# Kernel optimization log

Measured on AMD Instinct MI355X. Metric: run time of the kernel, lower is better.

Reference implementation:

```python
import jax, jax.numpy as jnp
import numpy as np

B, C, H, W = 4, 512, 32, 32
NUM_HEADS, DIM_HEAD = 16, 32
DIM_ATTN = NUM_HEADS * DIM_HEAD  # 512
N = H * W


def setup_inputs() -> dict:
    key = jax.random.key(0)
    ks = jax.random.split(key, 6)
    s = 0.02
    return {
        "x": jax.random.normal(ks[0], (B, C, H, W), jnp.float32),
        "w_qkv": jax.random.normal(ks[1], (3 * DIM_ATTN, C), jnp.float32) * s,
        "b_qkv": jax.random.normal(ks[2], (3 * DIM_ATTN,), jnp.float32) * s,
        "w_proj": jax.random.normal(ks[3], (C, DIM_ATTN), jnp.float32) * s,
        "b_proj": jax.random.normal(ks[4], (C,), jnp.float32) * s,
        "shared_rel_pos": jax.random.normal(ks[5], (1, NUM_HEADS, N, N), jnp.float32) * s,
    }


def reference(x, w_qkv, b_qkv, w_proj, b_proj, shared_rel_pos):
    b, c, h, w = x.shape
    n = h * w
    scale = DIM_HEAD ** -0.5
    # 1x1 conv == per-pixel matmul over channels
    qkv = jnp.einsum('bchw,oc->bohw', x, w_qkv) + b_qkv[None, :, None, None]
    # [B, heads, 3*dh, N] -> chunk along dim 2 (matches torch .chunk(3, dim=2))
    qkv = qkv.reshape(b, NUM_HEADS, 3 * DIM_HEAD, n)
    q, k, v = jnp.split(qkv, 3, axis=2)          # each [B, heads, dh, N]
    attn = jnp.einsum('bhdi,bhdj->bhij', q, k) * scale  # q^T @ k
    attn = attn + shared_rel_pos
    attn = jax.nn.softmax(attn, axis=-1)
    out = jnp.einsum('bhdj,bhij->bhdi', v, attn)  # v @ attn^T, [B, heads, dh, N]
    out = out.reshape(b, NUM_HEADS * DIM_HEAD, h, w)
    out = jnp.einsum('bchw,oc->bohw', out, w_proj) + b_proj[None, :, None, None]
    return out
```

## Files before the change

### kernel.cpp

```cpp
#include <hip/hip_runtime.h>
#include <cstdint>
#include <cstddef>

#define BATCH 4
#define CIN   512
#define NPIX  1024
#define HEADS 16
#define DH    32
#define DATTN 512
#define O_QKV 1536

typedef unsigned short u16;
typedef __bf16 bf16x4 __attribute__((ext_vector_type(4)));
typedef __bf16 bf16x8 __attribute__((ext_vector_type(8)));
typedef float  f32x4  __attribute__((ext_vector_type(4)));

typedef const __attribute__((address_space(1))) void g1_t;
typedef __attribute__((address_space(3))) void l3_t;

#if defined(__has_builtin)
#if __has_builtin(__builtin_amdgcn_exp2f)
#define EXP2(x) __builtin_amdgcn_exp2f(x)
#endif
#endif
#ifndef EXP2
#define EXP2(x) __expf((x) * 0.6931471805599453f)
#endif

__device__ __forceinline__ u16 f2bf(float f) {
  unsigned u = __float_as_uint(f);
  u += 0x7fffu + ((u >> 16) & 1u);
  return (u16)(u >> 16);
}

__device__ __forceinline__ void gl_lds16(const void* gp, void* lp) {
  __builtin_amdgcn_global_load_lds((g1_t*)gp, (l3_t*)lp, 16, 0, 0);
}

__global__ __launch_bounds__(256) void prep_fused(const float* __restrict__ x,
                                                  const float* __restrict__ w1,
                                                  const float* __restrict__ w2,
                                                  u16* __restrict__ xt,
                                                  u16* __restrict__ o1,
                                                  u16* __restrict__ o2) {
  const int t = threadIdx.x;
  if (blockIdx.x < 512) {
    __shared__ float sT[64][65];
    const int q  = blockIdx.x;
    const int n0 = (q & 15) << 6;
    const int c0 = ((q >> 4) & 7) << 6;
    const int b  = q >> 7;
    const float* xb = x + ((size_t)b * CIN + c0) * NPIX + n0;
#pragma unroll
    for (int i = 0; i < 4; ++i) {
      int r   = i * 16 + (t >> 4);
      int col = (t & 15) << 2;
      float4 v = *reinterpret_cast<const float4*>(&xb[(size_t)r * NPIX + col]);
      sT[r][col + 0] = v.x; sT[r][col + 1] = v.y;
      sT[r][col + 2] = v.z; sT[r][col + 3] = v.w;
    }
    __syncthreads();
#pragma unroll
    for (int i = 0; i < 2; ++i) {
      int nl = t >> 2;
      int ch = (t & 3) + (i << 2);
      u16 tmp[8];
#pragma unroll
      for (int e = 0; e < 8; ++e) tmp[e] = f2bf(sT[(ch << 3) + e][nl]);
      *reinterpret_cast<uint4*>(&xt[((size_t)b * NPIX + n0 + nl) * CIN + c0 + (ch << 3)]) =
          *reinterpret_cast<uint4*>(tmp);
    }
  } else {
    const int idx = (blockIdx.x - 512) * 256 + t;
    const int n1 = (O_QKV * CIN) >> 2;
    float4 v = (idx < n1) ? reinterpret_cast<const float4*>(w1)[idx]
                          : reinterpret_cast<const float4*>(w2)[idx - n1];
    uint2 pk = make_uint2((unsigned)f2bf(v.x) | ((unsigned)f2bf(v.y) << 16),
                          (unsigned)f2bf(v.z) | ((unsigned)f2bf(v.w) << 16));
    if (idx < n1) reinterpret_cast<uint2*>(o1)[idx] = pk;
    else          reinterpret_cast<uint2*>(o2)[idx - n1] = pk;
  }
}

__global__ __launch_bounds__(256) void gemm_qkv_mfma(const u16* __restrict__ wq,
                                                     const u16* __restrict__ xt,
                                                     const float* __restrict__ bias,
                                                     u16* __restrict__ qt,
                                                     u16* __restrict__ kt,
                                                     u16* __restrict__ vt) {
  __shared__ __align__(16) u16 sA[96 * 64];
  __shared__ __align__(16) u16 sB[128 * 64];
  const int t  = threadIdx.x;
  const int w  = t >> 6, l = t & 63, g = l >> 4, ln = l & 15;
  const int n0 = blockIdx.x * 128;
  const int h  = blockIdx.y;
  const int b  = blockIdx.z;
  const int wm = w >> 1, wn = w & 1;

  const u16* wbase = wq + (size_t)h * 96 * CIN;
  const u16* xbase = xt + ((size_t)b * NPIX + n0) * CIN;

  f32x4 acc[3][4];
#pragma unroll
  for (int mi = 0; mi < 3; ++mi)
#pragma unroll
    for (int ni = 0; ni < 4; ++ni) acc[mi][ni] = {0.f, 0.f, 0.f, 0.f};

  for (int k0 = 0; k0 < CIN; k0 += 64) {
#pragma unroll
    for (int i = 0; i < 3; ++i) {
      int chunk = i * 256 + (w << 6) + l;
      gl_lds16(wbase + ((size_t)(chunk >> 3)) * CIN + k0 + ((chunk & 7) << 3),
               (char*)sA + i * 4096 + (w << 10));
    }
#pragma unroll
    for (int i = 0; i < 4; ++i) {
      int chunk = i * 256 + (w << 6) + l;
      gl_lds16(xbase + ((size_t)(chunk >> 3)) * CIN + k0 + ((chunk & 7) << 3),
               (char*)sB + i * 4096 + (w << 10));
    }
    __syncthreads();
#pragma unroll
    for (int kk = 0; kk < 64; kk += 32) {
      bf16x8 af[3], bfr[4];
#pragma unroll
      for (int mi = 0; mi < 3; ++mi)
        af[mi] = *reinterpret_cast<const bf16x8*>(&sA[(48 * wm + 16 * mi + ln) * 64 + kk + (g << 3)]);
#pragma unroll
      for (int ni = 0; ni < 4; ++ni)
        bfr[ni] = *reinterpret_cast<const bf16x8*>(&sB[((wn << 6) + (ni << 4) + ln) * 64 + kk + (g << 3)]);
#pragma unroll
      for (int mi = 0; mi < 3; ++mi)
#pragma unroll
        for (int ni = 0; ni < 4; ++ni)
          acc[mi][ni] = __builtin_amdgcn_mfma_f32_16x16x32_bf16(af[mi], bfr[ni], acc[mi][ni], 0, 0, 0);
    }
    __syncthreads();
  }

  const float QSC = 0.17677669529663687f * 1.4426950408889634f;
  const float* bh = bias + h * 96;
#pragma unroll
  for (int mi = 0; mi < 3; ++mi) {
    const int sec = 48 * wm + 16 * mi;
    const int rb  = sec + (g << 2);
    const float b0 = bh[rb + 0], b1 = bh[rb + 1], b2 = bh[rb + 2], b3 = bh[rb + 3];
#pragma unroll
    for (int ni = 0; ni < 4; ++ni) {
      const int n = n0 + (wn << 6) + (ni << 4) + ln;
      f32x4 a = acc[mi][ni];
      float v0 = a[0] + b0, v1 = a[1] + b1, v2 = a[2] + b2, v3 = a[3] + b3;
      if (sec < 32) { v0 *= QSC; v1 *= QSC; v2 *= QSC; v3 *= QSC; }
      u16 e0 = f2bf(v0), e1 = f2bf(v1), e2 = f2bf(v2), e3 = f2bf(v3);
      if (sec < 32) {
        const int d = sec + (g << 2);
        uint2 pk = make_uint2((unsigned)e0 | ((unsigned)e1 << 16),
                              (unsigned)e2 | ((unsigned)e3 << 16));
        *reinterpret_cast<uint2*>(&qt[(((size_t)(b * HEADS + h)) * NPIX + n) * DH + d]) = pk;
      } else if (sec < 64) {
        const int d = sec - 32 + (g << 2);
        uint2 pk = make_uint2((unsigned)e0 | ((unsigned)e1 << 16),
                              (unsigned)e2 | ((unsigned)e3 << 16));
        *reinterpret_cast<uint2*>(&kt[(((size_t)(b * HEADS + h)) * NPIX + n) * DH + d]) = pk;
      } else {
        const int d = sec - 64 + (g << 2);
        u16* vp = &vt[(((size_t)(b * HEADS + h)) * DH + d) * NPIX + n];
        vp[0] = e0; vp[NPIX] = e1; vp[2 * NPIX] = e2; vp[3 * NPIX] = e3;
      }
    }
  }
}

__global__ __launch_bounds__(512, 4) void attn_mfma(const u16* __restrict__ qt,
                                                    const u16* __restrict__ kt,
                                                    const u16* __restrict__ vt,
                                                    const float* __restrict__ rel,
                                                    u16* __restrict__ aout) {
  __shared__ __align__(16) u16 sK[2][2][2][2048];
  __shared__ __align__(16) u16 sV[2][2][2][2048];
  __shared__ __align__(16) u16 sP[8][1024];

  const int t  = threadIdx.x;
  const int w  = t >> 6, l = t & 63, g = l >> 4, ln = l & 15;
  const int bid = blockIdx.x;
  const int xcd = bid & 7, sl = bid >> 3;
  const int bp  = sl & 1;
  const int i0  = ((sl >> 1) & 15) << 6;
  const int h   = (xcd << 1) | (sl >> 5);
  const int iw  = w & 3;
  const int jh  = w >> 2;

  const size_t bh0 = (size_t)((bp * 2 + 0) * HEADS + h);
  const size_t bh1 = (size_t)((bp * 2 + 1) * HEADS + h);

  const int sb2  = iw >> 1;
  const bool isK = (iw & 1) == 0;
  const size_t sbh = sb2 ? bh1 : bh0;
  const u16* src[4];
#pragma unroll
  for (int i = 0; i < 4; ++i) {
    const int c = i * 64 + l;
    const int r = c >> 3, slot = c & 7;
    if (isK) {
      const int kc = slot ^ (r & 7) ^ ((r >> 3) & 1);
      src[i] = kt + sbh * NPIX * DH +
               ((size_t)((jh << 9) + ((r << 1) | (kc >> 2)))) * DH + ((kc & 3) << 3);
    } else {
      const int vc = slot ^ (r & 7);
      src[i] = vt + (sbh * DH + r) * NPIX + (jh << 9) + (vc << 3);
    }
  }
  char* dstBase = isK ? (char*)&sK[0][jh][sb2][0] : (char*)&sV[0][jh][sb2][0];
  const size_t sstep = isK ? 2048 : 64;

#define STAGE(s_, p_) do {                                                   \
    gl_lds16(src[0] + (size_t)(s_) * sstep, dstBase + (p_) * 16384);         \
    gl_lds16(src[1] + (size_t)(s_) * sstep, dstBase + (p_) * 16384 + 1024);  \
    gl_lds16(src[2] + (size_t)(s_) * sstep, dstBase + (p_) * 16384 + 2048);  \
    gl_lds16(src[3] + (size_t)(s_) * sstep, dstBase + (p_) * 16384 + 3072);  \
  } while (0)

  STAGE(0, 0);

  bf16x8 qf0 = *reinterpret_cast<const bf16x8*>(
      qt + (bh0 * NPIX + i0 + (iw << 4) + ln) * DH + (g << 3));
  bf16x8 qf1 = *reinterpret_cast<const bf16x8*>(
      qt + (bh1 * NPIX + i0 + (iw << 4) + ln) * DH + (g << 3));

  const float* relp = rel + ((size_t)h * NPIX + i0 + (iw << 4) + (g << 2)) * NPIX +
                      (jh << 9) + (ln << 2);
  f32x4 relA4[4], relB4[4];
#pragma unroll
  for (int v = 0; v < 4; ++v)
    relA4[v] = *reinterpret_cast<const f32x4*>(relp + (size_t)v * NPIX);

  f32x4 vzero = {0.f, 0.f, 0.f, 0.f};
  f32x4 accO0[2] = {vzero, vzero};
  f32x4 accO1[2] = {vzero, vzero};
  f32x4 l_lane0 = vzero, l_lane1 = vzero;

  u16* sPw = &sP[w][0];
  const float LOG2E = 1.4426950408889634f;

  for (int s = 0; s < 8; ++s) {
    const int p = s & 1;
    __syncthreads();
    if (s < 7) {
      STAGE(s + 1, p ^ 1);
#pragma unroll
      for (int v = 0; v < 4; ++v)
        relB4[v] = *reinterpret_cast<const f32x4*>(relp + (size_t)v * NPIX + ((s + 1) << 6));
    }

#pragma unroll
    for (int b2 = 0; b2 < 2; ++b2) {
      const u16* Kb = &sK[p][jh][b2][0];
      const u16* Vb = &sV[p][jh][b2][0];
      const bf16x8 qf = b2 ? qf1 : qf0;

      f32x4 sfr[4];
      __builtin_amdgcn_s_setprio(1);
#pragma unroll
      for (int jj = 0; jj < 4; ++jj) {
        const int r  = (ln << 1) + (jj >> 1);
        const int ks = ((((jj & 1) << 2) | g) ^ (r & 7)) ^ ((r >> 3) & 1);
        bf16x8 kf = *reinterpret_cast<const bf16x8*>(Kb + r * 64 + ks * 8);
        sfr[jj] = __builtin_amdgcn_mfma_f32_16x16x32_bf16(qf, kf, vzero, 0, 0, 0);
      }
      __builtin_amdgcn_s_setprio(0);

#pragma unroll
      for (int v = 0; v < 4; ++v) {
        float p0 = EXP2(fmaf(relA4[v][0], LOG2E, sfr[0][v]));
        float p1 = EXP2(fmaf(relA4[v][1], LOG2E, sfr[1][v]));
        float p2 = EXP2(fmaf(relA4[v][2], LOG2E, sfr[2][v]));
        float p3 = EXP2(fmaf(relA4[v][3], LOG2E, sfr[3][v]));
        if (b2) l_lane1[v] += (p0 + p1) + (p2 + p3);
        else    l_lane0[v] += (p0 + p1) + (p2 + p3);
        bf16x4 pk;
        pk[0] = (__bf16)p0; pk[1] = (__bf16)p1; pk[2] = (__bf16)p2; pk[3] = (__bf16)p3;
        const int rw = (g << 2) + v;
        *reinterpret_cast<bf16x4*>(
            sPw + rw * 64 + ((((ln >> 1) ^ (rw & 7)) << 3) | ((ln & 1) << 2))) = pk;
      }

      __builtin_amdgcn_s_setprio(1);
#pragma unroll
      for (int kc = 0; kc < 2; ++kc) {
        const int lc = (kc << 2) | g;
        bf16x8 pa = *reinterpret_cast<const bf16x8*>(sPw + ln * 64 + ((lc ^ (ln & 7)) << 3));
#pragma unroll
        for (int dc = 0; dc < 2; ++dc) {
          const int d  = (dc << 4) + ln;
          const int vs = lc ^ (d & 7);
          bf16x8 vf = *reinterpret_cast<const bf16x8*>(Vb + d * 64 + vs * 8);
          if (b2) accO1[dc] = __builtin_amdgcn_mfma_f32_16x16x32_bf16(pa, vf, accO1[dc], 0, 0, 0);
          else    accO0[dc] = __builtin_amdgcn_mfma_f32_16x16x32_bf16(pa, vf, accO0[dc], 0, 0, 0);
        }
      }
      __builtin_amdgcn_s_setprio(0);
    }

    if (s < 7) {
#pragma unroll
      for (int v = 0; v < 4; ++v) relA4[v] = relB4[v];
    }
  }
#undef STAGE

  __syncthreads();
  float* mrg = (float*)&sK[0][0][0][0];
  if (jh == 1) {
    float* mp = mrg + ((size_t)((iw << 6) + l)) * 24;
    *reinterpret_cast<f32x4*>(mp +  0) = accO0[0];
    *reinterpret_cast<f32x4*>(mp +  4) = accO0[1];
    *reinterpret_cast<f32x4*>(mp +  8) = l_lane0;
    *reinterpret_cast<f32x4*>(mp + 12) = accO1[0];
    *reinterpret_cast<f32x4*>(mp + 16) = accO1[1];
    *reinterpret_cast<f32x4*>(mp + 20) = l_lane1;
  }
  __syncthreads();
  if (jh == 0) {
    const float* mp = mrg + ((size_t)((iw << 6) + l)) * 24;
    f32x4 o00 = accO0[0] + *reinterpret_cast<const f32x4*>(mp + 0);
    f32x4 o01 = accO0[1] + *reinterpret_cast<const f32x4*>(mp + 4);
    f32x4 lv0 = l_lane0 + *reinterpret_cast<const f32x4*>(mp + 8);
    f32x4 o10 = accO1[0] + *reinterpret_cast<const f32x4*>(mp + 12);
    f32x4 o11 = accO1[1] + *reinterpret_cast<const f32x4*>(mp + 16);
    f32x4 lv1 = l_lane1 + *reinterpret_cast<const f32x4*>(mp + 20);
#pragma unroll
    for (int v = 0; v < 4; ++v) {
      float ls = lv0[v];
      ls += __shfl_xor(ls, 1);
      ls += __shfl_xor(ls, 2);
      ls += __shfl_xor(ls, 4);
      ls += __shfl_xor(ls, 8);
      const float inv = 1.f / ls;
      const size_t row = (size_t)(bp * 2 + 0) * NPIX + i0 + (iw << 4) + (g << 2) + v;
      aout[row * DATTN + (h << 5) + ln]      = f2bf(o00[v] * inv);
      aout[row * DATTN + (h << 5) + 16 + ln] = f2bf(o01[v] * inv);
    }
#pragma unroll
    for (int v = 0; v < 4; ++v) {
      float ls = lv1[v];
      ls += __shfl_xor(ls, 1);
      ls += __shfl_xor(ls, 2);
      ls += __shfl_xor(ls, 4);
      ls += __shfl_xor(ls, 8);
      const float inv = 1.f / ls;
      const size_t row = (size_t)(bp * 2 + 1) * NPIX + i0 + (iw << 4) + (g << 2) + v;
      aout[row * DATTN + (h << 5) + ln]      = f2bf(o10[v] * inv);
      aout[row * DATTN + (h << 5) + 16 + ln] = f2bf(o11[v] * inv);
    }
  }
}

__global__ __launch_bounds__(256) void gemm_proj_mfma(const u16* __restrict__ wp,
                                                      const u16* __restrict__ at,
                                                      const float* __restrict__ bias,
                                                      float* __restrict__ out) {
  __shared__ __align__(16) u16 sA[64 * 64];
  __shared__ __align__(16) u16 sB[128 * 64];
  const int t  = threadIdx.x;
  const int w  = t >> 6, l = t & 63, g = l >> 4, ln = l & 15;
  const int n0 = blockIdx.x * 128;
  const int o0 = blockIdx.y * 64;
  const int b  = blockIdx.z;
  const int wm = w >> 1, wn = w & 1;

  const u16* wbase = wp + (size_t)o0 * DATTN;
  const u16* abase = at + ((size_t)b * NPIX + n0) * DATTN;

  f32x4 acc[2][4];
#pragma unroll
  for (int mi = 0; mi < 2; ++mi)
#pragma unroll
    for (int ni = 0; ni < 4; ++ni) acc[mi][ni] = {0.f, 0.f, 0.f, 0.f};

  for (int k0 = 0; k0 < DATTN; k0 += 64) {
#pragma unroll
    for (int i = 0; i < 2; ++i) {
      int chunk = i * 256 + (w << 6) + l;
      gl_lds16(wbase + ((size_t)(chunk >> 3)) * DATTN + k0 + ((chunk & 7) << 3),
               (char*)sA + i * 4096 + (w << 10));
    }
#pragma unroll
    for (int i = 0; i < 4; ++i) {
      int chunk = i * 256 + (w << 6) + l;
      gl_lds16(abase + ((size_t)(chunk >> 3)) * DATTN + k0 + ((chunk & 7) << 3),
               (char*)sB + i * 4096 + (w << 10));
    }
    __syncthreads();
#pragma unroll
    for (int kk = 0; kk < 64; kk += 32) {
      bf16x8 af[2], bfr[4];
#pragma unroll
      for (int mi = 0; mi < 2; ++mi)
        af[mi] = *reinterpret_cast<const bf16x8*>(&sA[((wm << 5) + (mi << 4) + ln) * 64 + kk + (g << 3)]);
#pragma unroll
      for (int ni = 0; ni < 4; ++ni)
        bfr[ni] = *reinterpret_cast<const bf16x8*>(&sB[((wn << 6) + (ni << 4) + ln) * 64 + kk + (g << 3)]);
#pragma unroll
      for (int mi = 0; mi < 2; ++mi)
#pragma unroll
        for (int ni = 0; ni < 4; ++ni)
          acc[mi][ni] = __builtin_amdgcn_mfma_f32_16x16x32_bf16(af[mi], bfr[ni], acc[mi][ni], 0, 0, 0);
    }
    __syncthreads();
  }

#pragma unroll
  for (int mi = 0; mi < 2; ++mi) {
    const int o = o0 + (wm << 5) + (mi << 4) + (g << 2);
    const float b0 = bias[o], b1 = bias[o + 1], b2 = bias[o + 2], b3 = bias[o + 3];
#pragma unroll
    for (int ni = 0; ni < 4; ++ni) {
      const int n = n0 + (wn << 6) + (ni << 4) + ln;
      float* op = &out[((size_t)b * DATTN + o) * NPIX + n];
      op[0]        = acc[mi][ni][0] + b0;
      op[NPIX]     = acc[mi][ni][1] + b1;
      op[2 * NPIX] = acc[mi][ni][2] + b2;
      op[3 * NPIX] = acc[mi][ni][3] + b3;
    }
  }
}

extern "C" void kernel_launch(void* const* d_in, const int* in_sizes, int n_in,
                              void* d_out, int out_size, void* d_ws, size_t ws_size,
                              hipStream_t stream) {
  (void)in_sizes; (void)n_in; (void)out_size; (void)ws_size;
  const float* x      = (const float*)d_in[0];
  const float* w_qkv  = (const float*)d_in[1];
  const float* b_qkv  = (const float*)d_in[2];
  const float* w_proj = (const float*)d_in[3];
  const float* b_proj = (const float*)d_in[4];
  const float* rel    = (const float*)d_in[5];
  float* out = (float*)d_out;

  u16* xt    = (u16*)d_ws;
  u16* wq_bf = xt + (size_t)BATCH * NPIX * CIN;
  u16* wp_bf = wq_bf + (size_t)O_QKV * CIN;
  u16* qt    = wp_bf + (size_t)DATTN * DATTN;
  u16* kt    = qt + (size_t)BATCH * HEADS * NPIX * DH;
  u16* vt    = kt + (size_t)BATCH * HEADS * NPIX * DH;
  u16* aout  = vt + (size_t)BATCH * HEADS * NPIX * DH;

  prep_fused<<<1536, 256, 0, stream>>>(x, w_qkv, w_proj, xt, wq_bf, wp_bf);
  gemm_qkv_mfma<<<dim3(NPIX / 128, HEADS, BATCH), 256, 0, stream>>>(wq_bf, xt, b_qkv, qt, kt, vt);
  attn_mfma<<<512, 512, 0, stream>>>(qt, kt, vt, rel, aout);
  gemm_proj_mfma<<<dim3(NPIX / 128, DATTN / 64, BATCH), 256, 0, stream>>>(wp_bf, aout, b_proj, out);
}
```

Baseline: 58.60 us.

## Process all four batches per attention block to reuse relative-position bias loads

Each attention block now handles all four batch items for a given head and query tile instead of two, so the fp32 shared_rel_pos tile is loaded once and reused across four batches. Grid halves to 256 blocks, LDS for K/V doubles, and launch bounds drop to two blocks per CU. Rel-pos traffic, the dominant global read, is halved. In exchange each CU holds fewer resident blocks, and 256 blocks may underfill the GPU's compute units.

```diff
diff --git a/kernel.cpp b/kernel.cpp
--- a/kernel.cpp
+++ b/kernel.cpp
@@ -171,61 +171,58 @@
   }
 }
 
-__global__ __launch_bounds__(512, 4) void attn_mfma(const u16* __restrict__ qt,
+__global__ __launch_bounds__(512, 2) void attn_mfma(const u16* __restrict__ qt,
                                                     const u16* __restrict__ kt,
                                                     const u16* __restrict__ vt,
                                                     const float* __restrict__ rel,
                                                     u16* __restrict__ aout) {
-  __shared__ __align__(16) u16 sK[2][2][2][2048];
-  __shared__ __align__(16) u16 sV[2][2][2][2048];
+  __shared__ __align__(16) u16 sK[2][2][4][2048];
+  __shared__ __align__(16) u16 sV[2][2][4][2048];
   __shared__ __align__(16) u16 sP[8][1024];
 
   const int t  = threadIdx.x;
   const int w  = t >> 6, l = t & 63, g = l >> 4, ln = l & 15;
   const int bid = blockIdx.x;
   const int xcd = bid & 7, sl = bid >> 3;
-  const int bp  = sl & 1;
-  const int i0  = ((sl >> 1) & 15) << 6;
-  const int h   = (xcd << 1) | (sl >> 5);
+  const int h   = (xcd << 1) | (sl >> 4);
+  const int i0  = (sl & 15) << 6;
   const int iw  = w & 3;
   const int jh  = w >> 2;
 
-  const size_t bh0 = (size_t)((bp * 2 + 0) * HEADS + h);
-  const size_t bh1 = (size_t)((bp * 2 + 1) * HEADS + h);
-
-  const int sb2  = iw >> 1;
-  const bool isK = (iw & 1) == 0;
-  const size_t sbh = sb2 ? bh1 : bh0;
-  const u16* src[4];
+  const size_t sbh = (size_t)(iw * HEADS + h);
+  const u16* ksrc[4];
+  const u16* vsrc[4];
 #pragma unroll
   for (int i = 0; i < 4; ++i) {
     const int c = i * 64 + l;
     const int r = c >> 3, slot = c & 7;
-    if (isK) {
-      const int kc = slot ^ (r & 7) ^ ((r >> 3) & 1);
-      src[i] = kt + sbh * NPIX * DH +
-               ((size_t)((jh << 9) + ((r << 1) | (kc >> 2)))) * DH + ((kc & 3) << 3);
-    } else {
-      const int vc = slot ^ (r & 7);
-      src[i] = vt + (sbh * DH + r) * NPIX + (jh << 9) + (vc << 3);
-    }
-  }
-  char* dstBase = isK ? (char*)&sK[0][jh][sb2][0] : (char*)&sV[0][jh][sb2][0];
-  const size_t sstep = isK ? 2048 : 64;
-
-#define STAGE(s_, p_) do {                                                   \
-    gl_lds16(src[0] + (size_t)(s_) * sstep, dstBase + (p_) * 16384);         \
-    gl_lds16(src[1] + (size_t)(s_) * sstep, dstBase + (p_) * 16384 + 1024);  \
-    gl_lds16(src[2] + (size_t)(s_) * sstep, dstBase + (p_) * 16384 + 2048);  \
-    gl_lds16(src[3] + (size_t)(s_) * sstep, dstBase + (p_) * 16384 + 3072);  \
+    const int kc = slot ^ (r & 7) ^ ((r >> 3) & 1);
+    ksrc[i] = kt + sbh * NPIX * DH +
+              ((size_t)((jh << 9) + ((r << 1) | (kc >> 2)))) * DH + ((kc & 3) << 3);
+    const int vc = slot ^ (r & 7);
+    vsrc[i] = vt + (sbh * DH + r) * NPIX + (jh << 9) + (vc << 3);
+  }
+  char* kdst = (char*)&sK[0][jh][iw][0];
+  char* vdst = (char*)&sV[0][jh][iw][0];
+
+#define STAGE(s_, p_) do {                                                    \
+    gl_lds16(ksrc[0] + (size_t)(s_) * 2048, kdst + (p_) * 32768);             \
+    gl_lds16(ksrc[1] + (size_t)(s_) * 2048, kdst + (p_) * 32768 + 1024);      \
+    gl_lds16(ksrc[2] + (size_t)(s_) * 2048, kdst + (p_) * 32768 + 2048);      \
+    gl_lds16(ksrc[3] + (size_t)(s_) * 2048, kdst + (p_) * 32768 + 3072);      \
+    gl_lds16(vsrc[0] + (size_t)(s_) * 64,   vdst + (p_) * 32768);             \
+    gl_lds16(vsrc[1] + (size_t)(s_) * 64,   vdst + (p_) * 32768 + 1024);      \
+    gl_lds16(vsrc[2] + (size_t)(s_) * 64,   vdst + (p_) * 32768 + 2048);      \
+    gl_lds16(vsrc[3] + (size_t)(s_) * 64,   vdst + (p_) * 32768 + 3072);      \
   } while (0)
 
   STAGE(0, 0);
 
-  bf16x8 qf0 = *reinterpret_cast<const bf16x8*>(
-      qt + (bh0 * NPIX + i0 + (iw << 4) + ln) * DH + (g << 3));
-  bf16x8 qf1 = *reinterpret_cast<const bf16x8*>(
-      qt + (bh1 * NPIX + i0 + (iw << 4) + ln) * DH + (g << 3));
+  bf16x8 qf[4];
+#pragma unroll
+  for (int b = 0; b < 4; ++b)
+    qf[b] = *reinterpret_cast<const bf16x8*>(
+        qt + (((size_t)(b * HEADS + h)) * NPIX + i0 + (iw << 4) + ln) * DH + (g << 3));
 
   const float* relp = rel + ((size_t)h * NPIX + i0 + (iw << 4) + (g << 2)) * NPIX +
                       (jh << 9) + (ln << 2);
@@ -235,9 +232,12 @@
     relA4[v] = *reinterpret_cast<const f32x4*>(relp + (size_t)v * NPIX);
 
   f32x4 vzero = {0.f, 0.f, 0.f, 0.f};
-  f32x4 accO0[2] = {vzero, vzero};
-  f32x4 accO1[2] = {vzero, vzero};
-  f32x4 l_lane0 = vzero, l_lane1 = vzero;
+  f32x4 accO[4][2];
+  f32x4 l_lane[4];
+#pragma unroll
+  for (int b = 0; b < 4; ++b) {
+    accO[b][0] = vzero; accO[b][1] = vzero; l_lane[b] = vzero;
+  }
 
   u16* sPw = &sP[w][0];
   const float LOG2E = 1.4426950408889634f;
@@ -253,10 +253,9 @@
     }
 
 #pragma unroll
-    for (int b2 = 0; b2 < 2; ++b2) {
+    for (int b2 = 0; b2 < 4; ++b2) {
       const u16* Kb = &sK[p][jh][b2][0];
       const u16* Vb = &sV[p][jh][b2][0];
-      const bf16x8 qf = b2 ? qf1 : qf0;
 
       f32x4 sfr[4];
       __builtin_amdgcn_s_setprio(1);
@@ -265,7 +264,7 @@
         const int r  = (ln << 1) + (jj >> 1);
         const int ks = ((((jj & 1) << 2) | g) ^ (r & 7)) ^ ((r >> 3) & 1);
         bf16x8 kf = *reinterpret_cast<const bf16x8*>(Kb + r * 64 + ks * 8);
-        sfr[jj] = __builtin_amdgcn_mfma_f32_16x16x32_bf16(qf, kf, vzero, 0, 0, 0);
+        sfr[jj] = __builtin_amdgcn_mfma_f32_16x16x32_bf16(qf[b2], kf, vzero, 0, 0, 0);
       }
       __builtin_amdgcn_s_setprio(0);
 
@@ -275,8 +274,7 @@
         float p1 = EXP2(fmaf(relA4[v][1], LOG2E, sfr[1][v]));
         float p2 = EXP2(fmaf(relA4[v][2], LOG2E, sfr[2][v]));
         float p3 = EXP2(fmaf(relA4[v][3], LOG2E, sfr[3][v]));
-        if (b2) l_lane1[v] += (p0 + p1) + (p2 + p3);
-        else    l_lane0[v] += (p0 + p1) + (p2 + p3);
+        l_lane[b2][v] += (p0 + p1) + (p2 + p3);
         bf16x4 pk;
         pk[0] = (__bf16)p0; pk[1] = (__bf16)p1; pk[2] = (__bf16)p2; pk[3] = (__bf16)p3;
         const int rw = (g << 2) + v;
@@ -294,8 +292,7 @@
           const int d  = (dc << 4) + ln;
           const int vs = lc ^ (d & 7);
           bf16x8 vf = *reinterpret_cast<const bf16x8*>(Vb + d * 64 + vs * 8);
-          if (b2) accO1[dc] = __builtin_amdgcn_mfma_f32_16x16x32_bf16(pa, vf, accO1[dc], 0, 0, 0);
-          else    accO0[dc] = __builtin_amdgcn_mfma_f32_16x16x32_bf16(pa, vf, accO0[dc], 0, 0, 0);
+          accO[b2][dc] = __builtin_amdgcn_mfma_f32_16x16x32_bf16(pa, vf, accO[b2][dc], 0, 0, 0);
         }
       }
       __builtin_amdgcn_s_setprio(0);
@@ -311,46 +308,34 @@
   __syncthreads();
   float* mrg = (float*)&sK[0][0][0][0];
   if (jh == 1) {
-    float* mp = mrg + ((size_t)((iw << 6) + l)) * 24;
-    *reinterpret_cast<f32x4*>(mp +  0) = accO0[0];
-    *reinterpret_cast<f32x4*>(mp +  4) = accO0[1];
-    *reinterpret_cast<f32x4*>(mp +  8) = l_lane0;
-    *reinterpret_cast<f32x4*>(mp + 12) = accO1[0];
-    *reinterpret_cast<f32x4*>(mp + 16) = accO1[1];
-    *reinterpret_cast<f32x4*>(mp + 20) = l_lane1;
+    float* mp = mrg + ((size_t)((iw << 6) + l)) * 48;
+#pragma unroll
+    for (int b = 0; b < 4; ++b) {
+      *reinterpret_cast<f32x4*>(mp + b * 12 + 0) = accO[b][0];
+      *reinterpret_cast<f32x4*>(mp + b * 12 + 4) = accO[b][1];
+      *reinterpret_cast<f32x4*>(mp + b * 12 + 8) = l_lane[b];
+    }
   }
   __syncthreads();
   if (jh == 0) {
-    const float* mp = mrg + ((size_t)((iw << 6) + l)) * 24;
-    f32x4 o00 = accO0[0] + *reinterpret_cast<const f32x4*>(mp + 0);
-    f32x4 o01 = accO0[1] + *reinterpret_cast<const f32x4*>(mp + 4);
-    f32x4 lv0 = l_lane0 + *reinterpret_cast<const f32x4*>(mp + 8);
-    f32x4 o10 = accO1[0] + *reinterpret_cast<const f32x4*>(mp + 12);
-    f32x4 o11 = accO1[1] + *reinterpret_cast<const f32x4*>(mp + 16);
-    f32x4 lv1 = l_lane1 + *reinterpret_cast<const f32x4*>(mp + 20);
-#pragma unroll
-    for (int v = 0; v < 4; ++v) {
-      float ls = lv0[v];
-      ls += __shfl_xor(ls, 1);
-      ls += __shfl_xor(ls, 2);
-      ls += __shfl_xor(ls, 4);
-      ls += __shfl_xor(ls, 8);
-      const float inv = 1.f / ls;
-      const size_t row = (size_t)(bp * 2 + 0) * NPIX + i0 + (iw << 4) + (g << 2) + v;
-      aout[row * DATTN + (h << 5) + ln]      = f2bf(o00[v] * inv);
-      aout[row * DATTN + (h << 5) + 16 + ln] = f2bf(o01[v] * inv);
-    }
-#pragma unroll
-    for (int v = 0; v < 4; ++v) {
-      float ls = lv1[v];
-      ls += __shfl_xor(ls, 1);
-      ls += __shfl_xor(ls, 2);
-      ls += __shfl_xor(ls, 4);
-      ls += __shfl_xor(ls, 8);
-      const float inv = 1.f / ls;
-      const size_t row = (size_t)(bp * 2 + 1) * NPIX + i0 + (iw << 4) + (g << 2) + v;
-      aout[row * DATTN + (h << 5) + ln]      = f2bf(o10[v] * inv);
-      aout[row * DATTN + (h << 5) + 16 + ln] = f2bf(o11[v] * inv);
+    const float* mp = mrg + ((size_t)((iw << 6) + l)) * 48;
+#pragma unroll
+    for (int b = 0; b < 4; ++b) {
+      f32x4 o0 = accO[b][0] + *reinterpret_cast<const f32x4*>(mp + b * 12 + 0);
+      f32x4 o1 = accO[b][1] + *reinterpret_cast<const f32x4*>(mp + b * 12 + 4);
+      f32x4 lv = l_lane[b] + *reinterpret_cast<const f32x4*>(mp + b * 12 + 8);
+#pragma unroll
+      for (int v = 0; v < 4; ++v) {
+        float ls = lv[v];
+        ls += __shfl_xor(ls, 1);
+        ls += __shfl_xor(ls, 2);
+        ls += __shfl_xor(ls, 4);
+        ls += __shfl_xor(ls, 8);
+        const float inv = 1.f / ls;
+        const size_t row = (size_t)b * NPIX + i0 + (iw << 4) + (g << 2) + v;
+        aout[row * DATTN + (h << 5) + ln]      = f2bf(o0[v] * inv);
+        aout[row * DATTN + (h << 5) + 16 + ln] = f2bf(o1[v] * inv);
+      }
     }
   }
 }
@@ -447,6 +432,6 @@
 
   prep_fused<<<1536, 256, 0, stream>>>(x, w_qkv, w_proj, xt, wq_bf, wp_bf);
   gemm_qkv_mfma<<<dim3(NPIX / 128, HEADS, BATCH), 256, 0, stream>>>(wq_bf, xt, b_qkv, qt, kt, vt);
-  attn_mfma<<<512, 512, 0, stream>>>(qt, kt, vt, rel, aout);
+  attn_mfma<<<256, 512, 0, stream>>>(qt, kt, vt, rel, aout);
   gemm_proj_mfma<<<dim3(NPIX / 128, DATTN / 64, BATCH), 256, 0, stream>>>(wp_bf, aout, b_proj, out);
 }
```

New measurement: 65.51 us. 11.8% more time.
